# Optimization experiments

Hardware: AMD Instinct MI355X
Metric: run time of the kernel (lower is better)

The kernel has to match this reference:

```python
import jax, jax.numpy as jnp
import numpy as np

HIDDEN = 1024
HEADS = 16
HEAD = HIDDEN // HEADS


def setup_inputs() -> dict:
    key = jax.random.key(0)
    ks = jax.random.split(key, 10)
    s = 1.0 / np.sqrt(HIDDEN)
    inp = {
        "x": jax.random.normal(ks[0], (2, 2048, HIDDEN), dtype=jnp.float32),
        "Wq": jax.random.uniform(ks[1], (HIDDEN, HIDDEN), jnp.float32, -s, s),
        "bq": jnp.zeros((HIDDEN,), jnp.float32),
        "Wk": jax.random.uniform(ks[2], (HIDDEN, HIDDEN), jnp.float32, -s, s),
        "bk": jnp.zeros((HIDDEN,), jnp.float32),
        "Wv": jax.random.uniform(ks[3], (HIDDEN, HIDDEN), jnp.float32, -s, s),
        "bv": jnp.zeros((HIDDEN,), jnp.float32),
        "Wo": jax.random.uniform(ks[4], (HIDDEN, HIDDEN), jnp.float32, -s, s),
        "bo": jnp.zeros((HIDDEN,), jnp.float32),
        "ln_g": jnp.ones((HIDDEN,), jnp.float32),
        "ln_b": jnp.zeros((HIDDEN,), jnp.float32),
    }
    return inp


def reference(x, Wq, bq, Wk, bk, Wv, bv, Wo, bo, ln_g, ln_b):
    B, S, H = x.shape
    # pre-LN (eps=1e-5 like torch LayerNorm)
    mu = jnp.mean(x, axis=-1, keepdims=True)
    var = jnp.mean(jnp.square(x - mu), axis=-1, keepdims=True)
    xn = (x - mu) * jax.lax.rsqrt(var + 1e-5) * ln_g + ln_b
    # QKV projections (torch Linear: x @ W.T + b) -> [B,S,heads,head]
    q = (xn @ Wq.T + bq).reshape(B, S, HEADS, HEAD)
    k = (xn @ Wk.T + bk).reshape(B, S, HEADS, HEAD)
    v = (xn @ Wv.T + bv).reshape(B, S, HEADS, HEAD)
    # scaled dot-product attention, naive full scores [B,heads,S,S]
    scores = jnp.einsum("bqhd,bkhd->bhqk", q, k) / jnp.sqrt(jnp.float32(HEAD))
    attn = jax.nn.softmax(scores, axis=-1)
    ctx = jnp.einsum("bhqk,bkhd->bqhd", attn, v).reshape(B, S, H)
    out = ctx @ Wo.T + bo
    return x + out  # dropout is identity in eval
```

## Files before the change

### kernel.cpp

```cpp
#include <hip/hip_runtime.h>
#include <hip/hip_bf16.h>
#include <stdint.h>

#define HID 1024
#define SEQ 2048
#define BATCH 2
#define NHEADS 16
#define HEADDIM 64
#define MROWS (BATCH*SEQ)

#define GAS __attribute__((address_space(1)))
#define LAS __attribute__((address_space(3)))

typedef __attribute__((ext_vector_type(8))) __bf16 bf16x8;
typedef __attribute__((ext_vector_type(4))) float f32x4;
typedef __attribute__((ext_vector_type(16))) float f32x16;

__device__ __forceinline__ ushort f2bf(float f) {
  union { float f; uint32_t u; } v; v.f = f;
  return (ushort)((v.u + 0x7FFFu + ((v.u >> 16) & 1u)) >> 16);
}

__device__ __forceinline__ void gl_lds16(const void* g, void* l) {
  __builtin_amdgcn_global_load_lds((const GAS void*)g, (LAS void*)l, 16, 0, 0);
}

__device__ __forceinline__ uint32_t cvtpk(float a, float b) {
  uint32_t r;
  asm("v_cvt_pk_bf16_f32 %0, %1, %2" : "=v"(r) : "v"(a), "v"(b));
  return r;
}

__device__ __forceinline__ void pl32swap(uint32_t& a, uint32_t& b) {
  asm("v_permlane32_swap_b32 %0, %1" : "+v"(a), "+v"(b));
}

__global__ __launch_bounds__(256) void k_cvt(const float* __restrict__ Wq,
                                             const float* __restrict__ Wk,
                                             const float* __restrict__ Wv,
                                             const float* __restrict__ Wo,
                                             ushort* __restrict__ dst) {
  int mat = blockIdx.y;
  const float* src = (mat == 0) ? Wq : (mat == 1) ? Wk : (mat == 2) ? Wv : Wo;
  int off = (blockIdx.x * 256 + threadIdx.x) * 4;
  float4 v = *(const float4*)(src + off);
  ushort4 o;
  o.x = f2bf(v.x); o.y = f2bf(v.y); o.z = f2bf(v.z); o.w = f2bf(v.w);
  *(ushort4*)(dst + (size_t)mat * (HID * HID) + off) = o;
}

__global__ __launch_bounds__(256) void k_ln(const float* __restrict__ x,
                                            const float* __restrict__ g,
                                            const float* __restrict__ b,
                                            ushort* __restrict__ xn) {
  int row = blockIdx.x;
  int t = threadIdx.x;
  const float* xr = x + (size_t)row * HID;
  float4 v = *(const float4*)(xr + t * 4);
  float s = v.x + v.y + v.z + v.w;
  float s2 = v.x * v.x + v.y * v.y + v.z * v.z + v.w * v.w;
  for (int m = 1; m < 64; m <<= 1) { s += __shfl_xor(s, m); s2 += __shfl_xor(s2, m); }
  __shared__ float ws[4], ws2[4];
  int wid = t >> 6;
  if ((t & 63) == 0) { ws[wid] = s; ws2[wid] = s2; }
  __syncthreads();
  s = ws[0] + ws[1] + ws[2] + ws[3];
  s2 = ws2[0] + ws2[1] + ws2[2] + ws2[3];
  float mu = s * (1.0f / HID);
  float var = s2 * (1.0f / HID) - mu * mu;
  float rstd = rsqrtf(var + 1e-5f);
  float4 gg = *(const float4*)(g + t * 4);
  float4 bb = *(const float4*)(b + t * 4);
  ushort4 o;
  o.x = f2bf((v.x - mu) * rstd * gg.x + bb.x);
  o.y = f2bf((v.y - mu) * rstd * gg.y + bb.y);
  o.z = f2bf((v.z - mu) * rstd * gg.z + bb.z);
  o.w = f2bf((v.w - mu) * rstd * gg.w + bb.w);
  *(ushort4*)(xn + (size_t)row * HID + t * 4) = o;
}

__global__ __launch_bounds__(256) void k_qkv(const ushort* __restrict__ xn,
                                             const ushort* __restrict__ wmat,
                                             const float* __restrict__ bq,
                                             const float* __restrict__ bk,
                                             const float* __restrict__ bv,
                                             ushort* __restrict__ qo,
                                             ushort* __restrict__ ko,
                                             ushort* __restrict__ vo) {
  __shared__ ushort As[128 * 32];
  __shared__ ushort Bs[128 * 32];
  int tid = threadIdx.x;
  int lane = tid & 63;
  int wv = tid >> 6;
  int quad = lane >> 4;
  int l16 = lane & 15;
  int m0 = blockIdx.x * 128;
  int ng = blockIdx.y * 128;
  int mat = ng >> 10;
  int nloc = ng & 1023;
  const ushort* wptr = wmat + (size_t)mat * (HID * HID) + (size_t)nloc * HID;
  const float* bias = (mat == 0) ? bq : (mat == 1) ? bk : bv;
  ushort* outp = (mat == 0) ? qo : (mat == 1) ? ko : vo;
  const float scl = (mat == 0) ? 0.18033688011112042f : 1.0f;

  int arow = tid >> 2;
  int acol = (tid & 3) * 8;
  int wm = (wv >> 1) * 64, wn = (wv & 1) * 64;

  f32x4 acc[4][4] = {};
  for (int k0 = 0; k0 < HID; k0 += 32) {
    __syncthreads();
    for (int t = 0; t < 2; t++) {
      gl_lds16(xn + (size_t)(m0 + t * 64 + arow) * HID + k0 + acol,
               As + t * 2048 + wv * 512);
      gl_lds16(wptr + (size_t)(t * 64 + arow) * HID + k0 + acol,
               Bs + t * 2048 + wv * 512);
    }
    __syncthreads();
    bf16x8 af[4], bfr[4];
    for (int i = 0; i < 4; i++)
      af[i] = *(const bf16x8*)&As[(wm + i * 16 + l16) * 32 + quad * 8];
    for (int n = 0; n < 4; n++)
      bfr[n] = *(const bf16x8*)&Bs[(wn + n * 16 + l16) * 32 + quad * 8];
    for (int i = 0; i < 4; i++)
      for (int n = 0; n < 4; n++)
        acc[i][n] = __builtin_amdgcn_mfma_f32_16x16x32_bf16(af[i], bfr[n], acc[i][n], 0, 0, 0);
  }
  float bv4[4];
  for (int n = 0; n < 4; n++) bv4[n] = bias[nloc + wn + n * 16 + l16];
  for (int i = 0; i < 4; i++) {
    int mrow = m0 + wm + i * 16 + quad * 4;
    for (int n = 0; n < 4; n++) {
      int col = nloc + wn + n * 16 + l16;
      int h = col >> 6, d = col & 63;
      for (int r = 0; r < 4; r++) {
        int m = mrow + r;
        int bidx = m >> 11, sidx = m & 2047;
        size_t dst;
        if (mat == 2)
          dst = (((size_t)(bidx * NHEADS + h) * HEADDIM) + d) * SEQ + sidx;
        else
          dst = (((size_t)(bidx * NHEADS + h) * SEQ) + sidx) * HEADDIM + d;
        outp[dst] = f2bf((acc[i][n][r] + bv4[n]) * scl);
      }
    }
  }
}

__global__ __launch_bounds__(256, 2) void k_attn(const ushort* __restrict__ Q,
                                                 const ushort* __restrict__ K,
                                                 const ushort* __restrict__ Vt,
                                                 ushort* __restrict__ ctx) {
  __shared__ ushort Ksm[2][64 * 64];
  __shared__ ushort Vsm[2][64 * 64];
  int tid = threadIdx.x, lane = tid & 63, wv = tid >> 6;
  int l32 = lane & 31, hi = lane >> 5;
  int bh = blockIdx.y;
  int q0 = blockIdx.x * 128;
  const ushort* Qb = Q + ((size_t)bh * SEQ + q0 + wv * 32 + l32) * HEADDIM;
  const ushort* Kb = K + (size_t)bh * SEQ * HEADDIM;
  const ushort* Vb = Vt + (size_t)bh * HEADDIM * SEQ;

  bf16x8 qf[4];
#pragma unroll
  for (int f = 0; f < 4; f++)
    qf[f] = *(const bf16x8*)(Qb + f * 16 + hi * 8);

  bf16x8 ones;
#pragma unroll
  for (int j = 0; j < 8; j++) ones[j] = (__bf16)1.0f;

  int gsl = lane & 7;
  int rowA = wv * 8 + (lane >> 3);
  int rowB = 32 + wv * 8 + (lane >> 3);
  const ushort* kSrcA = Kb + rowA * HEADDIM + ((gsl ^ (rowA & 7)) * 8);
  const ushort* kSrcB = Kb + rowB * HEADDIM + ((gsl ^ (rowB & 7)) * 8);
  const ushort* vSrcA = Vb + (size_t)rowA * SEQ + ((gsl ^ (rowA & 7)) * 8);
  const ushort* vSrcB = Vb + (size_t)rowB * SEQ + ((gsl ^ (rowB & 7)) * 8);
  int ldsA = wv * 512;
  int ldsB = 2048 + wv * 512;

  f32x16 Oa0 = {}, Oa1 = {}, Os = {};
  int rsw = (l32 & 7);

  gl_lds16(kSrcA, &Ksm[0][ldsA]);
  gl_lds16(kSrcB, &Ksm[0][ldsB]);
  gl_lds16(vSrcA, &Vsm[0][ldsA]);
  gl_lds16(vSrcB, &Vsm[0][ldsB]);
  __syncthreads();

  for (int kt = 0; kt < SEQ / 64; kt++) {
    int buf = kt & 1;
    if (kt + 1 < SEQ / 64) {
      int nb = buf ^ 1;
      size_t ko = (size_t)(kt + 1) * 64 * HEADDIM;
      size_t vo = (size_t)(kt + 1) * 64;
      gl_lds16(kSrcA + ko, &Ksm[nb][ldsA]);
      gl_lds16(kSrcB + ko, &Ksm[nb][ldsB]);
      gl_lds16(vSrcA + vo, &Vsm[nb][ldsA]);
      gl_lds16(vSrcB + vo, &Vsm[nb][ldsB]);
    }

    f32x16 s0 = {}, s1 = {};
    __builtin_amdgcn_s_setprio(1);
#pragma unroll
    for (int f = 0; f < 4; f++) {
      int g = 2 * f + hi;
      bf16x8 k0 = *(const bf16x8*)&Ksm[buf][l32 * 64 + ((g ^ rsw) * 8)];
      bf16x8 k1 = *(const bf16x8*)&Ksm[buf][(32 + l32) * 64 + ((g ^ rsw) * 8)];
      s0 = __builtin_amdgcn_mfma_f32_32x32x16_bf16(k0, qf[f], s0, 0, 0, 0);
      s1 = __builtin_amdgcn_mfma_f32_32x32x16_bf16(k1, qf[f], s1, 0, 0, 0);
    }
    __builtin_amdgcn_s_setprio(0);

    union { uint32_t u[4]; bf16x8 v; } pf0, pf1, pf2, pf3;
    {
      uint32_t c0 = cvtpk(__builtin_amdgcn_exp2f(fminf(s0[0], 80.f)),
                          __builtin_amdgcn_exp2f(fminf(s0[1], 80.f)));
      uint32_t c1 = cvtpk(__builtin_amdgcn_exp2f(fminf(s0[2], 80.f)),
                          __builtin_amdgcn_exp2f(fminf(s0[3], 80.f)));
      uint32_t c2 = cvtpk(__builtin_amdgcn_exp2f(fminf(s0[4], 80.f)),
                          __builtin_amdgcn_exp2f(fminf(s0[5], 80.f)));
      uint32_t c3 = cvtpk(__builtin_amdgcn_exp2f(fminf(s0[6], 80.f)),
                          __builtin_amdgcn_exp2f(fminf(s0[7], 80.f)));
      uint32_t c4 = cvtpk(__builtin_amdgcn_exp2f(fminf(s0[8], 80.f)),
                          __builtin_amdgcn_exp2f(fminf(s0[9], 80.f)));
      uint32_t c5 = cvtpk(__builtin_amdgcn_exp2f(fminf(s0[10], 80.f)),
                          __builtin_amdgcn_exp2f(fminf(s0[11], 80.f)));
      uint32_t c6 = cvtpk(__builtin_amdgcn_exp2f(fminf(s0[12], 80.f)),
                          __builtin_amdgcn_exp2f(fminf(s0[13], 80.f)));
      uint32_t c7 = cvtpk(__builtin_amdgcn_exp2f(fminf(s0[14], 80.f)),
                          __builtin_amdgcn_exp2f(fminf(s0[15], 80.f)));
      pl32swap(c0, c2); pl32swap(c1, c3); pl32swap(c4, c6); pl32swap(c5, c7);
      pf0.u[0] = c0; pf0.u[1] = c1; pf0.u[2] = c2; pf0.u[3] = c3;
      pf1.u[0] = c4; pf1.u[1] = c5; pf1.u[2] = c6; pf1.u[3] = c7;
    }
    {
      uint32_t c0 = cvtpk(__builtin_amdgcn_exp2f(fminf(s1[0], 80.f)),
                          __builtin_amdgcn_exp2f(fminf(s1[1], 80.f)));
      uint32_t c1 = cvtpk(__builtin_amdgcn_exp2f(fminf(s1[2], 80.f)),
                          __builtin_amdgcn_exp2f(fminf(s1[3], 80.f)));
      uint32_t c2 = cvtpk(__builtin_amdgcn_exp2f(fminf(s1[4], 80.f)),
                          __builtin_amdgcn_exp2f(fminf(s1[5], 80.f)));
      uint32_t c3 = cvtpk(__builtin_amdgcn_exp2f(fminf(s1[6], 80.f)),
                          __builtin_amdgcn_exp2f(fminf(s1[7], 80.f)));
      uint32_t c4 = cvtpk(__builtin_amdgcn_exp2f(fminf(s1[8], 80.f)),
                          __builtin_amdgcn_exp2f(fminf(s1[9], 80.f)));
      uint32_t c5 = cvtpk(__builtin_amdgcn_exp2f(fminf(s1[10], 80.f)),
                          __builtin_amdgcn_exp2f(fminf(s1[11], 80.f)));
      uint32_t c6 = cvtpk(__builtin_amdgcn_exp2f(fminf(s1[12], 80.f)),
                          __builtin_amdgcn_exp2f(fminf(s1[13], 80.f)));
      uint32_t c7 = cvtpk(__builtin_amdgcn_exp2f(fminf(s1[14], 80.f)),
                          __builtin_amdgcn_exp2f(fminf(s1[15], 80.f)));
      pl32swap(c0, c2); pl32swap(c1, c3); pl32swap(c4, c6); pl32swap(c5, c7);
      pf2.u[0] = c0; pf2.u[1] = c1; pf2.u[2] = c2; pf2.u[3] = c3;
      pf3.u[0] = c4; pf3.u[1] = c5; pf3.u[2] = c6; pf3.u[3] = c7;
    }

    __builtin_amdgcn_s_setprio(1);
#pragma unroll
    for (int kf = 0; kf < 4; kf++) {
      int g = 2 * kf + hi;
      bf16x8 pv = (kf == 0) ? pf0.v : (kf == 1) ? pf1.v : (kf == 2) ? pf2.v : pf3.v;
      bf16x8 v0 = *(const bf16x8*)&Vsm[buf][l32 * 64 + ((g ^ rsw) * 8)];
      bf16x8 v1 = *(const bf16x8*)&Vsm[buf][(32 + l32) * 64 + ((g ^ rsw) * 8)];
      Oa0 = __builtin_amdgcn_mfma_f32_32x32x16_bf16(pv, v0, Oa0, 0, 0, 0);
      Oa1 = __builtin_amdgcn_mfma_f32_32x32x16_bf16(pv, v1, Oa1, 0, 0, 0);
      Os  = __builtin_amdgcn_mfma_f32_32x32x16_bf16(pv, ones, Os, 0, 0, 0);
    }
    __builtin_amdgcn_s_setprio(0);

    __syncthreads();
  }

  int bidx = bh >> 4, h = bh & 15;
#pragma unroll
  for (int r = 0; r < 16; r++) {
    float inv = 1.0f / Os[r];
    int qloc = (r & 3) + 8 * (r >> 2) + 4 * hi;
    int sidx = q0 + wv * 32 + qloc;
    size_t base = ((size_t)(bidx * SEQ) + sidx) * HID + h * HEADDIM;
    ctx[base + l32]      = f2bf(Oa0[r] * inv);
    ctx[base + 32 + l32] = f2bf(Oa1[r] * inv);
  }
}

__global__ __launch_bounds__(256) void k_oproj(const ushort* __restrict__ ctx,
                                               const ushort* __restrict__ wmat,
                                               const float* __restrict__ bo,
                                               const float* __restrict__ x,
                                               float* __restrict__ out) {
  __shared__ ushort As[128 * 32];
  __shared__ ushort Bs[128 * 32];
  int tid = threadIdx.x;
  int lane = tid & 63;
  int wv = tid >> 6;
  int quad = lane >> 4;
  int l16 = lane & 15;
  int m0 = blockIdx.x * 128;
  int n0 = blockIdx.y * 128;
  const ushort* wptr = wmat + (size_t)3 * (HID * HID) + (size_t)n0 * HID;
  int arow = tid >> 2;
  int acol = (tid & 3) * 8;
  int wm = (wv >> 1) * 64, wn = (wv & 1) * 64;

  f32x4 acc[4][4] = {};
  for (int k0 = 0; k0 < HID; k0 += 32) {
    __syncthreads();
    for (int t = 0; t < 2; t++) {
      gl_lds16(ctx + (size_t)(m0 + t * 64 + arow) * HID + k0 + acol,
               As + t * 2048 + wv * 512);
      gl_lds16(wptr + (size_t)(t * 64 + arow) * HID + k0 + acol,
               Bs + t * 2048 + wv * 512);
    }
    __syncthreads();
    bf16x8 af[4], bfr[4];
    for (int i = 0; i < 4; i++)
      af[i] = *(const bf16x8*)&As[(wm + i * 16 + l16) * 32 + quad * 8];
    for (int n = 0; n < 4; n++)
      bfr[n] = *(const bf16x8*)&Bs[(wn + n * 16 + l16) * 32 + quad * 8];
    for (int i = 0; i < 4; i++)
      for (int n = 0; n < 4; n++)
        acc[i][n] = __builtin_amdgcn_mfma_f32_16x16x32_bf16(af[i], bfr[n], acc[i][n], 0, 0, 0);
  }
  float bv4[4];
  for (int n = 0; n < 4; n++) bv4[n] = bo[n0 + wn + n * 16 + l16];
  for (int i = 0; i < 4; i++) {
    int mrow = m0 + wm + i * 16 + quad * 4;
    for (int n = 0; n < 4; n++) {
      int col = n0 + wn + n * 16 + l16;
      for (int r = 0; r < 4; r++) {
        size_t idx = (size_t)(mrow + r) * HID + col;
        out[idx] = acc[i][n][r] + bv4[n] + x[idx];
      }
    }
  }
}

extern "C" void kernel_launch(void* const* d_in, const int* in_sizes, int n_in,
                              void* d_out, int out_size, void* d_ws, size_t ws_size,
                              hipStream_t stream) {
  const float* x    = (const float*)d_in[0];
  const float* Wq   = (const float*)d_in[1];
  const float* bq   = (const float*)d_in[2];
  const float* Wk   = (const float*)d_in[3];
  const float* bk   = (const float*)d_in[4];
  const float* Wv   = (const float*)d_in[5];
  const float* bv   = (const float*)d_in[6];
  const float* Wo   = (const float*)d_in[7];
  const float* bo   = (const float*)d_in[8];
  const float* ln_g = (const float*)d_in[9];
  const float* ln_b = (const float*)d_in[10];
  float* out = (float*)d_out;

  const size_t MB = 1024 * 1024;
  ushort* ws_w = (ushort*)d_ws;
  ushort* xn   = (ushort*)((char*)d_ws + 8 * MB);
  ushort* Qw   = (ushort*)((char*)d_ws + 16 * MB);
  ushort* Kw   = (ushort*)((char*)d_ws + 24 * MB);
  ushort* Vw   = (ushort*)((char*)d_ws + 32 * MB);
  ushort* Cw   = (ushort*)((char*)d_ws + 40 * MB);

  k_cvt<<<dim3(1024, 4), 256, 0, stream>>>(Wq, Wk, Wv, Wo, ws_w);
  k_ln<<<dim3(MROWS), 256, 0, stream>>>(x, ln_g, ln_b, xn);
  k_qkv<<<dim3(32, 24), 256, 0, stream>>>(xn, ws_w, bq, bk, bv, Qw, Kw, Vw);
  k_attn<<<dim3(SEQ / 128, BATCH * NHEADS), 256, 0, stream>>>(Qw, Kw, Vw, Cw);
  k_oproj<<<dim3(32, 8), 256, 0, stream>>>(Cw, ws_w, bo, x, out);
}
```

Measured before the change: 208.3 us.

## Software-pipeline attention loop: overlap QK^T of next tile with softmax/PV of previous

Restructures the attention K-tile loop so that each iteration computes QK^T scores for tile t while doing the exp/softmax conversion and PV MFMAs for tile t-1. V gets a triple-buffered LDS ring and the loop is unrolled by two with ping-pong score registers, plus a prologue and epilogue. The goal is to hide the exp/convert VALU latency behind MFMA work and give the scheduler independent instruction streams. In exchange it uses more registers (two sets of scores plus prefetched V fragments) and more LDS, which may strain the two-blocks-per-CU occupancy target.

```diff
diff --git a/kernel.cpp b/kernel.cpp
--- a/kernel.cpp
+++ b/kernel.cpp
@@ -147,12 +147,87 @@
   }
 }
 
+#define E2(x) __builtin_amdgcn_exp2f(fminf((x), 80.f))
+
+#define SOFTMAX_PF(S0, S1)                                                     \
+    union { uint32_t u[4]; bf16x8 v; } pf0, pf1, pf2, pf3;                     \
+    {                                                                          \
+      uint32_t c0 = cvtpk(E2(S0[0]),  E2(S0[1]));                              \
+      uint32_t c1 = cvtpk(E2(S0[2]),  E2(S0[3]));                              \
+      uint32_t c2 = cvtpk(E2(S0[4]),  E2(S0[5]));                              \
+      uint32_t c3 = cvtpk(E2(S0[6]),  E2(S0[7]));                              \
+      uint32_t c4 = cvtpk(E2(S0[8]),  E2(S0[9]));                              \
+      uint32_t c5 = cvtpk(E2(S0[10]), E2(S0[11]));                             \
+      uint32_t c6 = cvtpk(E2(S0[12]), E2(S0[13]));                             \
+      uint32_t c7 = cvtpk(E2(S0[14]), E2(S0[15]));                             \
+      pl32swap(c0, c2); pl32swap(c1, c3); pl32swap(c4, c6); pl32swap(c5, c7);  \
+      pf0.u[0] = c0; pf0.u[1] = c1; pf0.u[2] = c2; pf0.u[3] = c3;              \
+      pf1.u[0] = c4; pf1.u[1] = c5; pf1.u[2] = c6; pf1.u[3] = c7;              \
+    }                                                                          \
+    {                                                                          \
+      uint32_t c0 = cvtpk(E2(S1[0]),  E2(S1[1]));                              \
+      uint32_t c1 = cvtpk(E2(S1[2]),  E2(S1[3]));                              \
+      uint32_t c2 = cvtpk(E2(S1[4]),  E2(S1[5]));                              \
+      uint32_t c3 = cvtpk(E2(S1[6]),  E2(S1[7]));                              \
+      uint32_t c4 = cvtpk(E2(S1[8]),  E2(S1[9]));                              \
+      uint32_t c5 = cvtpk(E2(S1[10]), E2(S1[11]));                             \
+      uint32_t c6 = cvtpk(E2(S1[12]), E2(S1[13]));                             \
+      uint32_t c7 = cvtpk(E2(S1[14]), E2(S1[15]));                             \
+      pl32swap(c0, c2); pl32swap(c1, c3); pl32swap(c4, c6); pl32swap(c5, c7);  \
+      pf2.u[0] = c0; pf2.u[1] = c1; pf2.u[2] = c2; pf2.u[3] = c3;              \
+      pf3.u[0] = c4; pf3.u[1] = c5; pf3.u[2] = c6; pf3.u[3] = c7;              \
+    }
+
+#define ATTN_BODY(T, SC0, SC1, SP0, SP1, DO_DMA)                               \
+  do {                                                                         \
+    if (DO_DMA) {                                                              \
+      size_t ko = (size_t)((T) + 1) * 64 * HEADDIM;                            \
+      size_t vo = (size_t)((T) + 1) * 64;                                      \
+      int kn = kc ^ 1;                                                         \
+      gl_lds16(kSrcA + ko, &Ksm[kn][ldsA]);                                    \
+      gl_lds16(kSrcB + ko, &Ksm[kn][ldsB]);                                    \
+      gl_lds16(vSrcA + vo, &Vsm[vn][ldsA]);                                    \
+      gl_lds16(vSrcB + vo, &Vsm[vn][ldsB]);                                    \
+    }                                                                          \
+    SC0 = (f32x16){}; SC1 = (f32x16){};                                        \
+    __builtin_amdgcn_s_setprio(1);                                             \
+    _Pragma("unroll")                                                          \
+    for (int f = 0; f < 4; f++) {                                              \
+      int g = 2 * f + hi;                                                      \
+      bf16x8 k0 = *(const bf16x8*)&Ksm[kc][l32 * 64 + ((g ^ rsw) * 8)];        \
+      bf16x8 k1 = *(const bf16x8*)&Ksm[kc][(32 + l32) * 64 + ((g ^ rsw) * 8)]; \
+      SC0 = __builtin_amdgcn_mfma_f32_32x32x16_bf16(k0, qf[f], SC0, 0, 0, 0);  \
+      SC1 = __builtin_amdgcn_mfma_f32_32x32x16_bf16(k1, qf[f], SC1, 0, 0, 0);  \
+    }                                                                          \
+    __builtin_amdgcn_s_setprio(0);                                             \
+    bf16x8 vf[8];                                                              \
+    _Pragma("unroll")                                                          \
+    for (int kf = 0; kf < 4; kf++) {                                           \
+      int g = 2 * kf + hi;                                                     \
+      vf[2 * kf]     = *(const bf16x8*)&Vsm[vp][l32 * 64 + ((g ^ rsw) * 8)];   \
+      vf[2 * kf + 1] = *(const bf16x8*)&Vsm[vp][(32 + l32) * 64 + ((g ^ rsw) * 8)]; \
+    }                                                                          \
+    SOFTMAX_PF(SP0, SP1)                                                       \
+    __builtin_amdgcn_s_setprio(1);                                             \
+    _Pragma("unroll")                                                          \
+    for (int kf = 0; kf < 4; kf++) {                                           \
+      bf16x8 pv = (kf == 0) ? pf0.v : (kf == 1) ? pf1.v : (kf == 2) ? pf2.v : pf3.v; \
+      Oa0 = __builtin_amdgcn_mfma_f32_32x32x16_bf16(pv, vf[2 * kf], Oa0, 0, 0, 0);   \
+      Oa1 = __builtin_amdgcn_mfma_f32_32x32x16_bf16(pv, vf[2 * kf + 1], Oa1, 0, 0, 0); \
+      Os  = __builtin_amdgcn_mfma_f32_32x32x16_bf16(pv, ones, Os, 0, 0, 0);    \
+    }                                                                          \
+    __builtin_amdgcn_s_setprio(0);                                             \
+    __syncthreads();                                                           \
+    if (DO_DMA) kc ^= 1;                                                       \
+    { int tmp = vp; vp = vc; vc = vn; vn = tmp; }                              \
+  } while (0)
+
 __global__ __launch_bounds__(256, 2) void k_attn(const ushort* __restrict__ Q,
                                                  const ushort* __restrict__ K,
                                                  const ushort* __restrict__ Vt,
                                                  ushort* __restrict__ ctx) {
   __shared__ ushort Ksm[2][64 * 64];
-  __shared__ ushort Vsm[2][64 * 64];
+  __shared__ ushort Vsm[3][64 * 64];
   int tid = threadIdx.x, lane = tid & 63, wv = tid >> 6;
   int l32 = lane & 31, hi = lane >> 5;
   int bh = blockIdx.y;
@@ -181,6 +256,7 @@
   int ldsB = 2048 + wv * 512;
 
   f32x16 Oa0 = {}, Oa1 = {}, Os = {};
+  f32x16 sA0, sA1, sB0, sB1;
   int rsw = (l32 & 7);
 
   gl_lds16(kSrcA, &Ksm[0][ldsA]);
@@ -189,88 +265,52 @@
   gl_lds16(vSrcB, &Vsm[0][ldsB]);
   __syncthreads();
 
-  for (int kt = 0; kt < SEQ / 64; kt++) {
-    int buf = kt & 1;
-    if (kt + 1 < SEQ / 64) {
-      int nb = buf ^ 1;
-      size_t ko = (size_t)(kt + 1) * 64 * HEADDIM;
-      size_t vo = (size_t)(kt + 1) * 64;
-      gl_lds16(kSrcA + ko, &Ksm[nb][ldsA]);
-      gl_lds16(kSrcB + ko, &Ksm[nb][ldsB]);
-      gl_lds16(vSrcA + vo, &Vsm[nb][ldsA]);
-      gl_lds16(vSrcB + vo, &Vsm[nb][ldsB]);
-    }
-
-    f32x16 s0 = {}, s1 = {};
+  {
+    size_t ko = (size_t)64 * HEADDIM;
+    size_t vo = (size_t)64;
+    gl_lds16(kSrcA + ko, &Ksm[1][ldsA]);
+    gl_lds16(kSrcB + ko, &Ksm[1][ldsB]);
+    gl_lds16(vSrcA + vo, &Vsm[1][ldsA]);
+    gl_lds16(vSrcB + vo, &Vsm[1][ldsB]);
+    sA0 = (f32x16){}; sA1 = (f32x16){};
     __builtin_amdgcn_s_setprio(1);
 #pragma unroll
     for (int f = 0; f < 4; f++) {
       int g = 2 * f + hi;
-      bf16x8 k0 = *(const bf16x8*)&Ksm[buf][l32 * 64 + ((g ^ rsw) * 8)];
-      bf16x8 k1 = *(const bf16x8*)&Ksm[buf][(32 + l32) * 64 + ((g ^ rsw) * 8)];
-      s0 = __builtin_amdgcn_mfma_f32_32x32x16_bf16(k0, qf[f], s0, 0, 0, 0);
-      s1 = __builtin_amdgcn_mfma_f32_32x32x16_bf16(k1, qf[f], s1, 0, 0, 0);
+      bf16x8 k0 = *(const bf16x8*)&Ksm[0][l32 * 64 + ((g ^ rsw) * 8)];
+      bf16x8 k1 = *(const bf16x8*)&Ksm[0][(32 + l32) * 64 + ((g ^ rsw) * 8)];
+      sA0 = __builtin_amdgcn_mfma_f32_32x32x16_bf16(k0, qf[f], sA0, 0, 0, 0);
+      sA1 = __builtin_amdgcn_mfma_f32_32x32x16_bf16(k1, qf[f], sA1, 0, 0, 0);
     }
     __builtin_amdgcn_s_setprio(0);
-
-    union { uint32_t u[4]; bf16x8 v; } pf0, pf1, pf2, pf3;
-    {
-      uint32_t c0 = cvtpk(__builtin_amdgcn_exp2f(fminf(s0[0], 80.f)),
-                          __builtin_amdgcn_exp2f(fminf(s0[1], 80.f)));
-      uint32_t c1 = cvtpk(__builtin_amdgcn_exp2f(fminf(s0[2], 80.f)),
-                          __builtin_amdgcn_exp2f(fminf(s0[3], 80.f)));
-      uint32_t c2 = cvtpk(__builtin_amdgcn_exp2f(fminf(s0[4], 80.f)),
-                          __builtin_amdgcn_exp2f(fminf(s0[5], 80.f)));
-      uint32_t c3 = cvtpk(__builtin_amdgcn_exp2f(fminf(s0[6], 80.f)),
-                          __builtin_amdgcn_exp2f(fminf(s0[7], 80.f)));
-      uint32_t c4 = cvtpk(__builtin_amdgcn_exp2f(fminf(s0[8], 80.f)),
-                          __builtin_amdgcn_exp2f(fminf(s0[9], 80.f)));
-      uint32_t c5 = cvtpk(__builtin_amdgcn_exp2f(fminf(s0[10], 80.f)),
-                          __builtin_amdgcn_exp2f(fminf(s0[11], 80.f)));
-      uint32_t c6 = cvtpk(__builtin_amdgcn_exp2f(fminf(s0[12], 80.f)),
-                          __builtin_amdgcn_exp2f(fminf(s0[13], 80.f)));
-      uint32_t c7 = cvtpk(__builtin_amdgcn_exp2f(fminf(s0[14], 80.f)),
-                          __builtin_amdgcn_exp2f(fminf(s0[15], 80.f)));
-      pl32swap(c0, c2); pl32swap(c1, c3); pl32swap(c4, c6); pl32swap(c5, c7);
-      pf0.u[0] = c0; pf0.u[1] = c1; pf0.u[2] = c2; pf0.u[3] = c3;
-      pf1.u[0] = c4; pf1.u[1] = c5; pf1.u[2] = c6; pf1.u[3] = c7;
-    }
-    {
-      uint32_t c0 = cvtpk(__builtin_amdgcn_exp2f(fminf(s1[0], 80.f)),
-                          __builtin_amdgcn_exp2f(fminf(s1[1], 80.f)));
-      uint32_t c1 = cvtpk(__builtin_amdgcn_exp2f(fminf(s1[2], 80.f)),
-                          __builtin_amdgcn_exp2f(fminf(s1[3], 80.f)));
-      uint32_t c2 = cvtpk(__builtin_amdgcn_exp2f(fminf(s1[4], 80.f)),
-                          __builtin_amdgcn_exp2f(fminf(s1[5], 80.f)));
-      uint32_t c3 = cvtpk(__builtin_amdgcn_exp2f(fminf(s1[6], 80.f)),
-                          __builtin_amdgcn_exp2f(fminf(s1[7], 80.f)));
-      uint32_t c4 = cvtpk(__builtin_amdgcn_exp2f(fminf(s1[8], 80.f)),
-                          __builtin_amdgcn_exp2f(fminf(s1[9], 80.f)));
-      uint32_t c5 = cvtpk(__builtin_amdgcn_exp2f(fminf(s1[10], 80.f)),
-                          __builtin_amdgcn_exp2f(fminf(s1[11], 80.f)));
-      uint32_t c6 = cvtpk(__builtin_amdgcn_exp2f(fminf(s1[12], 80.f)),
-                          __builtin_amdgcn_exp2f(fminf(s1[13], 80.f)));
-      uint32_t c7 = cvtpk(__builtin_amdgcn_exp2f(fminf(s1[14], 80.f)),
-                          __builtin_amdgcn_exp2f(fminf(s1[15], 80.f)));
-      pl32swap(c0, c2); pl32swap(c1, c3); pl32swap(c4, c6); pl32swap(c5, c7);
-      pf2.u[0] = c0; pf2.u[1] = c1; pf2.u[2] = c2; pf2.u[3] = c3;
-      pf3.u[0] = c4; pf3.u[1] = c5; pf3.u[2] = c6; pf3.u[3] = c7;
-    }
-
-    __builtin_amdgcn_s_setprio(1);
+    __syncthreads();
+  }
+
+  int kc = 1, vp = 0, vc = 1, vn = 2;
+  for (int t = 1; t < 31; t += 2) {
+    ATTN_BODY(t,     sB0, sB1, sA0, sA1, true);
+    ATTN_BODY(t + 1, sA0, sA1, sB0, sB1, true);
+  }
+  ATTN_BODY(31, sB0, sB1, sA0, sA1, false);
+
+  {
+    bf16x8 vf[8];
 #pragma unroll
     for (int kf = 0; kf < 4; kf++) {
       int g = 2 * kf + hi;
+      vf[2 * kf]     = *(const bf16x8*)&Vsm[vp][l32 * 64 + ((g ^ rsw) * 8)];
+      vf[2 * kf + 1] = *(const bf16x8*)&Vsm[vp][(32 + l32) * 64 + ((g ^ rsw) * 8)];
+    }
+    SOFTMAX_PF(sB0, sB1)
+    __builtin_amdgcn_s_setprio(1);
+#pragma unroll
+    for (int kf = 0; kf < 4; kf++) {
       bf16x8 pv = (kf == 0) ? pf0.v : (kf == 1) ? pf1.v : (kf == 2) ? pf2.v : pf3.v;
-      bf16x8 v0 = *(const bf16x8*)&Vsm[buf][l32 * 64 + ((g ^ rsw) * 8)];
-      bf16x8 v1 = *(const bf16x8*)&Vsm[buf][(32 + l32) * 64 + ((g ^ rsw) * 8)];
-      Oa0 = __builtin_amdgcn_mfma_f32_32x32x16_bf16(pv, v0, Oa0, 0, 0, 0);
-      Oa1 = __builtin_amdgcn_mfma_f32_32x32x16_bf16(pv, v1, Oa1, 0, 0, 0);
+      Oa0 = __builtin_amdgcn_mfma_f32_32x32x16_bf16(pv, vf[2 * kf], Oa0, 0, 0, 0);
+      Oa1 = __builtin_amdgcn_mfma_f32_32x32x16_bf16(pv, vf[2 * kf + 1], Oa1, 0, 0, 0);
       Os  = __builtin_amdgcn_mfma_f32_32x32x16_bf16(pv, ones, Os, 0, 0, 0);
     }
     __builtin_amdgcn_s_setprio(0);
-
-    __syncthreads();
   }
 
   int bidx = bh >> 4, h = bh & 15;
```

After: 211.3 us. About the same (+1.5%).
